# Kernel optimization log

Measured on AMD Instinct MI355X. Metric: run time of the kernel, lower is better.

The kernel has to match this reference:

```python
import jax, jax.numpy as jnp
import numpy as np

K = 15.0          # sigmoid sharpness in get_approxi
THETA2 = 400.0    # gaussian 'theta2' parameter
LOSS_WEIGHT = 1.0


def obb2poly_le90(boxes):
    # boxes [..., 5] = (x, y, w, h, a) -> poly [..., 8]
    x, y, w, h, a = (boxes[..., i] for i in range(5))
    cosa, sina = jnp.cos(a), jnp.sin(a)
    wx, wy = 0.5 * w * cosa, 0.5 * w * sina
    hx, hy = -0.5 * h * sina, 0.5 * h * cosa
    return jnp.stack([
        x - wx - hx, y - wy - hy,
        x + wx - hx, y + wy - hy,
        x + wx + hx, y + wy + hy,
        x - wx + hx, y - wy + hy,
    ], axis=-1)


def setup_inputs() -> dict:
    key = jax.random.key(0)
    k1, k2, k3, k4, k5, k6 = jax.random.split(key, 6)
    N, M = 256, 512

    def make_boxes(k):
        u = jax.random.uniform(k, (N, 5), dtype=jnp.float32)
        cx = 100.0 + 300.0 * u[:, 0]
        cy = 100.0 + 300.0 * u[:, 1]
        w = 20.0 + 100.0 * u[:, 2]
        h = 20.0 + 100.0 * u[:, 3]
        a = (u[:, 4] - 0.5) * (jnp.pi / 2)
        return jnp.stack([cx, cy, w, h, a], axis=-1)

    pred = make_boxes(k1)
    target = make_boxes(k2)
    mask = 512.0 * jax.random.uniform(k3, (N, M, 2), dtype=jnp.float32)
    grad_x = jax.random.normal(k4, (N, M), dtype=jnp.float32)
    grad_y = jax.random.normal(k5, (N, M), dtype=jnp.float32)
    offset = 50.0 * jax.random.uniform(k6, (N, 2), dtype=jnp.float32)
    return {"pred": pred, "target": target, "mask": mask,
            "grad_x": grad_x, "grad_y": grad_y, "offset": offset}


def _my_loss(pred, target, mask, grad_x, grad_y, offset):
    # pred/target [N,5], mask [N,M,2], grad_x/grad_y [N,M], offset [N,2]
    px = pred[:, 0] - offset[:, 0]   # [N]
    py = pred[:, 1] - offset[:, 1]
    pw, ph, pa = pred[:, 2], pred[:, 3], pred[:, 4]
    gx = target[:, 0] - offset[:, 0]
    gy = target[:, 1] - offset[:, 1]
    gw, gh, ga = target[:, 2], target[:, 3], target[:, 4]

    mx, my = mask[..., 0], mask[..., 1]            # [N,M]
    dx = mx - gx[:, None]
    dy = my - gy[:, None]
    d = jnp.sqrt(dx * dx + dy * dy)                # [N,M]
    acos_arg = jnp.clip((gx[:, None] - mx) / d, -1.0, 1.0)
    acosv = jnp.arccos(acos_arg)
    beta = jnp.where(gy[:, None] >= my, ga[:, None] + acosv, ga[:, None] - acosv)

    d_w = jnp.abs(d * jnp.cos(beta))
    d_h = jnp.abs(d * jnp.sin(beta))
    sig = jax.nn.sigmoid
    approxi_1 = (1.0 - sig(K * (d_w - gw[:, None]) / gw[:, None])) * \
                (1.0 - sig(K * (d_h - gh[:, None]) / gh[:, None]))  # [N,M]

    d_w_p = pw[:, None] * d_w / gw[:, None]
    d_h_p = ph[:, None] * d_h / gh[:, None]
    zeros = jnp.zeros_like(d_w_p)
    boxes = jnp.stack([zeros, zeros, 2.0 * d_w_p, 2.0 * d_h_p,
                       jnp.broadcast_to(pa[:, None], d_w_p.shape)], axis=-1)
    pts = obb2poly_le90(boxes)                     # [N,M,8]

    half_pi = jnp.pi / 2
    q2 = (beta > -half_pi) & (beta <= 0.0)
    q3 = (beta > -jnp.pi) & (beta <= -half_pi)
    q4 = (beta > half_pi) & (beta <= jnp.pi)
    # default (q1: 0 < beta <= pi/2) -> corner 0
    gpx = jnp.where(q2, pts[..., 2], jnp.where(q3, pts[..., 4], jnp.where(q4, pts[..., 6], pts[..., 0])))
    gpy = jnp.where(q2, pts[..., 3], jnp.where(q3, pts[..., 5], jnp.where(q4, pts[..., 7], pts[..., 1])))
    guass_x = px[:, None] + gpx                    # [N,M]
    guass_y = py[:, None] + gpy

    # approxi_2[n,i,j] = exp(+||guass_i - mask_j||^2 / (2*theta2^2)) / (2*pi*theta2)
    dgx = guass_x[:, :, None] - mx[:, None, :]
    dgy = guass_y[:, :, None] - my[:, None, :]
    approxi_2 = jnp.exp((dgx * dgx + dgy * dgy) / (2.0 * THETA2 * THETA2)) / (2.0 * jnp.pi * THETA2)

    # w[n,i,j] = gx_i*gx_j + gy_i*gy_j
    w = grad_x[:, :, None] * grad_x[:, None, :] + grad_y[:, :, None] * grad_y[:, None, :]

    loss_per_box = jnp.mean(w * approxi_2 * approxi_1[:, None, :], axis=(1, 2))  # [N]
    return loss_per_box


def reference(pred, target, mask, grad_x, grad_y, offset):
    loss_per_box = _my_loss(pred, target, mask, grad_x, grad_y, offset)
    return LOSS_WEIGHT * jnp.mean(loss_per_box)  # reduction='mean'
```

## Files before the change

### kernel.cpp

```cpp
#include <hip/hip_runtime.h>
#include <math.h>

#define N_BOX 256
#define M_PTS 512
#define SPLIT 2

__global__ __launch_bounds__(256, 2) void loss_kernel(
    const float* __restrict__ pred,
    const float* __restrict__ target,
    const float* __restrict__ mask,
    const float* __restrict__ gradx,
    const float* __restrict__ grady,
    const float* __restrict__ offset,
    float* __restrict__ out)
{
    __shared__ float4 sPack[M_PTS];
    __shared__ float  sWave[4];

    const int n    = blockIdx.x & (N_BOX - 1);
    const int half = blockIdx.x >> 8;
    const int t    = threadIdx.x;

    const float offx = offset[n * 2 + 0];
    const float offy = offset[n * 2 + 1];
    const float px = pred[n * 5 + 0] - offx;
    const float py = pred[n * 5 + 1] - offy;
    const float pw = pred[n * 5 + 2];
    const float ph = pred[n * 5 + 3];
    const float pa = pred[n * 5 + 4];
    const float gx = target[n * 5 + 0] - offx;
    const float gy = target[n * 5 + 1] - offy;
    const float gw = target[n * 5 + 2];
    const float gh = target[n * 5 + 3];
    const float ga = target[n * 5 + 4];

    float sinpa, cospa;
    sincosf(pa, &sinpa, &cospa);

    const float KC       = 15.0f;
    const float THETA2   = 400.0f;
    const float inv_norm = 1.0f / (2.0f * (float)M_PI * THETA2);
    const float PI  = (float)M_PI;
    const float HPI = (float)M_PI * 0.5f;

    float G1x = 0.0f, G1y = 0.0f, g1x = 0.0f, g1y = 0.0f;
#pragma unroll
    for (int j = 0; j < 2; ++j) {
        const int m = t + j * 256;
        const float mx = mask[((size_t)n * M_PTS + m) * 2 + 0];
        const float my = mask[((size_t)n * M_PTS + m) * 2 + 1];
        const float dx = mx - gx;
        const float dy = my - gy;
        const float d  = sqrtf(dx * dx + dy * dy);
        float aa = (gx - mx) / d;
        aa = fminf(1.0f, fmaxf(-1.0f, aa));
        const float ac   = acosf(aa);
        const float beta = (gy >= my) ? (ga + ac) : (ga - ac);
        float sb, cb;
        sincosf(beta, &sb, &cb);
        const float d_w = fabsf(d * cb);
        const float d_h = fabsf(d * sb);
        const float s1  = 1.0f / (1.0f + expf(-(KC * (d_w - gw) / gw)));
        const float s2  = 1.0f / (1.0f + expf(-(KC * (d_h - gh) / gh)));
        const float a1  = (1.0f - s1) * (1.0f - s2);
        const float dwp = pw * d_w / gw;
        const float dhp = ph * d_h / gh;
        const float wx = dwp * cospa, wy = dwp * sinpa;
        const float hx = -dhp * sinpa, hy = dhp * cospa;
        float gpx, gpy;
        if (beta > -HPI && beta <= 0.0f)        { gpx =  wx - hx; gpy =  wy - hy; }
        else if (beta > -PI && beta <= -HPI)    { gpx =  wx + hx; gpy =  wy + hy; }
        else if (beta >  HPI && beta <=  PI)    { gpx = -wx + hx; gpy = -wy + hy; }
        else                                    { gpx = -wx - hx; gpy = -wy - hy; }
        const float gX  = px + gpx;
        const float gY  = py + gpy;
        const float gvx = gradx[(size_t)n * M_PTS + m];
        const float gvy = grady[(size_t)n * M_PTS + m];
        const float B   = a1 * inv_norm;
        sPack[m] = make_float4(mx, my, gvx * B, gvy * B);
        if (j == half) { G1x = gX; G1y = gY; g1x = gvx; g1y = gvy; }
    }
    __syncthreads();

    const float c1 = 1.4426950408889634f / (2.0f * THETA2 * THETA2);
    float acc = 0.0f;
#pragma unroll 8
    for (int m2 = 0; m2 < M_PTS; ++m2) {
        const float4 p = sPack[m2];
        const float dgx = G1x - p.x;
        const float dgy = G1y - p.y;
        const float s   = fmaf(dgy, dgy, dgx * dgx);
        const float e   = exp2f(s * c1);
        const float w   = fmaf(g1y, p.w, g1x * p.z);
        acc = fmaf(w, e, acc);
    }

#pragma unroll
    for (int off = 32; off > 0; off >>= 1)
        acc += __shfl_down(acc, off, 64);
    if ((t & 63) == 0) sWave[t >> 6] = acc;
    __syncthreads();
    if (t == 0) {
        const float tot = sWave[0] + sWave[1] + sWave[2] + sWave[3];
        const float scale = 1.0f / ((float)N_BOX * (float)M_PTS * (float)M_PTS);
        atomicAdd(out, tot * scale);
    }
}

extern "C" void kernel_launch(void* const* d_in, const int* in_sizes, int n_in,
                              void* d_out, int out_size, void* d_ws, size_t ws_size,
                              hipStream_t stream) {
    const float* pred   = (const float*)d_in[0];
    const float* target = (const float*)d_in[1];
    const float* mask   = (const float*)d_in[2];
    const float* gradx  = (const float*)d_in[3];
    const float* grady  = (const float*)d_in[4];
    const float* offset = (const float*)d_in[5];
    float* out = (float*)d_out;

    hipMemsetAsync(out, 0, sizeof(float), stream);
    hipLaunchKernelGGL(loss_kernel, dim3(N_BOX * SPLIT), dim3(256), 0, stream,
                       pred, target, mask, gradx, grady, offset, out);
}
```

Baseline: 93.79 us.

## Rewrite loss kernel with trig-free corner selection, register row tiling, two-stage reduction

Replaces the acos/sincos beta computation with an algebraic rotation into the target box frame plus sign logic for quadrant selection, and computes the sigmoid weights with hardware exp2. Each 64-thread block now keeps 8 rows per thread in packed float2 registers and streams one 64-column slice of the mask from shared memory, pre-scaling coordinates by sqrt(c1) so the multiply inside exp2 disappears. The grad-weighted products are factored out of the inner loop into two accumulators per row. The memset and atomicAdd are replaced by per-block partial sums in the workspace and a separate reduction kernel. This trades an extra launch and duplicated per-row prologue work across the 8 splits for far fewer transcendental calls and more register reuse, and the wrap-around quadrant logic may disagree with the original at boundary cases.

```diff
diff --git a/kernel.cpp b/kernel.cpp
--- a/kernel.cpp
+++ b/kernel.cpp
@@ -1,25 +1,30 @@
 #include <hip/hip_runtime.h>
 #include <math.h>
 
-#define N_BOX 256
-#define M_PTS 512
-#define SPLIT 2
+typedef float v2f __attribute__((ext_vector_type(2)));
 
-__global__ __launch_bounds__(256, 2) void loss_kernel(
+#define N_BOX   256
+#define M_PTS   512
+#define S_SPLIT 8
+#define BLK     64
+#define R_ROWS  8
+#define M2_PER  (M_PTS / S_SPLIT)
+#define GRID    (N_BOX * S_SPLIT)
+
+__global__ __launch_bounds__(BLK, 2) void loss_main(
     const float* __restrict__ pred,
     const float* __restrict__ target,
     const float* __restrict__ mask,
     const float* __restrict__ gradx,
     const float* __restrict__ grady,
     const float* __restrict__ offset,
-    float* __restrict__ out)
+    float* __restrict__ part)
 {
-    __shared__ float4 sPack[M_PTS];
-    __shared__ float  sWave[4];
+    __shared__ float4 sPack[M2_PER];
 
-    const int n    = blockIdx.x & (N_BOX - 1);
-    const int half = blockIdx.x >> 8;
-    const int t    = threadIdx.x;
+    const int n = blockIdx.x >> 3;
+    const int s = blockIdx.x & 7;
+    const int t = threadIdx.x;
 
     const float offx = offset[n * 2 + 0];
     const float offy = offset[n * 2 + 1];
@@ -34,76 +39,110 @@
     const float gh = target[n * 5 + 3];
     const float ga = target[n * 5 + 4];
 
-    float sinpa, cospa;
+    float sinpa, cospa, singa, cosga;
     sincosf(pa, &sinpa, &cospa);
+    sincosf(ga, &singa, &cosga);
 
-    const float KC       = 15.0f;
     const float THETA2   = 400.0f;
+    const float LOG2E    = 1.4426950408889634f;
+    const float c1       = LOG2E / (2.0f * THETA2 * THETA2);
+    const float rs       = sqrtf(c1);
     const float inv_norm = 1.0f / (2.0f * (float)M_PI * THETA2);
-    const float PI  = (float)M_PI;
-    const float HPI = (float)M_PI * 0.5f;
 
-    float G1x = 0.0f, G1y = 0.0f, g1x = 0.0f, g1y = 0.0f;
+    const float pwg = pw / gw, phg = ph / gh;
+    const float cwx = pwg * cospa, swx = pwg * sinpa;
+    const float chx = phg * cospa, shx = phg * sinpa;
+    const float absinga = fabsf(singa);
+    const float kA  = 15.0f * LOG2E / gw;
+    const float kH  = 15.0f * LOG2E / gh;
+    const float kB  = 15.0f * LOG2E;
+    const float pxrs = px * rs, pyrs = py * rs;
+    const bool  gaPos = (ga > 0.0f), gaNeg = (ga < 0.0f);
+
+    const float2* mask2 = (const float2*)mask;
+    const size_t  baseM = (size_t)n * M_PTS;
+
+    v2f Gx[4], Gy[4], gvx2[4], gvy2[4];
+
 #pragma unroll
-    for (int j = 0; j < 2; ++j) {
-        const int m = t + j * 256;
-        const float mx = mask[((size_t)n * M_PTS + m) * 2 + 0];
-        const float my = mask[((size_t)n * M_PTS + m) * 2 + 1];
-        const float dx = mx - gx;
-        const float dy = my - gy;
-        const float d  = sqrtf(dx * dx + dy * dy);
-        float aa = (gx - mx) / d;
-        aa = fminf(1.0f, fmaxf(-1.0f, aa));
-        const float ac   = acosf(aa);
-        const float beta = (gy >= my) ? (ga + ac) : (ga - ac);
-        float sb, cb;
-        sincosf(beta, &sb, &cb);
-        const float d_w = fabsf(d * cb);
-        const float d_h = fabsf(d * sb);
-        const float s1  = 1.0f / (1.0f + expf(-(KC * (d_w - gw) / gw)));
-        const float s2  = 1.0f / (1.0f + expf(-(KC * (d_h - gh) / gh)));
-        const float a1  = (1.0f - s1) * (1.0f - s2);
-        const float dwp = pw * d_w / gw;
-        const float dhp = ph * d_h / gh;
-        const float wx = dwp * cospa, wy = dwp * sinpa;
-        const float hx = -dhp * sinpa, hy = dhp * cospa;
-        float gpx, gpy;
-        if (beta > -HPI && beta <= 0.0f)        { gpx =  wx - hx; gpy =  wy - hy; }
-        else if (beta > -PI && beta <= -HPI)    { gpx =  wx + hx; gpy =  wy + hy; }
-        else if (beta >  HPI && beta <=  PI)    { gpx = -wx + hx; gpy = -wy + hy; }
-        else                                    { gpx = -wx - hx; gpy = -wy - hy; }
-        const float gX  = px + gpx;
-        const float gY  = py + gpy;
-        const float gvx = gradx[(size_t)n * M_PTS + m];
-        const float gvy = grady[(size_t)n * M_PTS + m];
-        const float B   = a1 * inv_norm;
-        sPack[m] = make_float4(mx, my, gvx * B, gvy * B);
-        if (j == half) { G1x = gX; G1y = gY; g1x = gvx; g1y = gvy; }
+    for (int r = 0; r < R_ROWS; ++r) {
+        const int    m  = t + (r << 6);
+        const float2 mp = mask2[baseM + m];
+        const float dx = mp.x - gx;
+        const float dy = mp.y - gy;
+        const float u = singa * dy - cosga * dx;
+        const float v = -(cosga * dy + singa * dx);
+        const bool sgaOk = gaPos ? (dy <= 0.0f) : (gaNeg ? (dy > 0.0f) : false);
+        const bool wrap  = sgaOk && (dx > 0.0f) && (dx * absinga > fabsf(dy) * cosga);
+        const float au = fabsf(u), av = fabsf(v);
+        const float dws = (wrap || v > 0.0f) ? -au : au;
+        const float dhs = (wrap || u > 0.0f) ? -av : av;
+        const float gpx = dws * cwx - dhs * shx;
+        const float gpy = dws * swx + dhs * chx;
+        const float gvx = gradx[baseM + m];
+        const float gvy = grady[baseM + m];
+        Gx[r >> 1][r & 1]   = fmaf(gpx, rs, pxrs);
+        Gy[r >> 1][r & 1]   = fmaf(gpy, rs, pyrs);
+        gvx2[r >> 1][r & 1] = gvx;
+        gvy2[r >> 1][r & 1] = gvy;
+        if (r == s) {
+            const float eA = __builtin_amdgcn_exp2f(fmaf(au, kA, -kB));
+            const float eB = __builtin_amdgcn_exp2f(fmaf(av, kH, -kB));
+            const float B  = inv_norm / ((1.0f + eA) * (1.0f + eB));
+            sPack[t] = make_float4(mp.x * rs, mp.y * rs, gvx * B, gvy * B);
+        }
     }
     __syncthreads();
 
-    const float c1 = 1.4426950408889634f / (2.0f * THETA2 * THETA2);
-    float acc = 0.0f;
-#pragma unroll 8
-    for (int m2 = 0; m2 < M_PTS; ++m2) {
+    v2f accz[4], accw[4];
+#pragma unroll
+    for (int q = 0; q < 4; ++q) { accz[q] = (v2f)0.0f; accw[q] = (v2f)0.0f; }
+
+#pragma unroll 4
+    for (int m2 = 0; m2 < M2_PER; ++m2) {
         const float4 p = sPack[m2];
-        const float dgx = G1x - p.x;
-        const float dgy = G1y - p.y;
-        const float s   = fmaf(dgy, dgy, dgx * dgx);
-        const float e   = exp2f(s * c1);
-        const float w   = fmaf(g1y, p.w, g1x * p.z);
-        acc = fmaf(w, e, acc);
+#pragma unroll
+        for (int q = 0; q < 4; ++q) {
+            v2f dgx = Gx[q] - p.x;
+            v2f dgy = Gy[q] - p.y;
+            v2f sa  = dgx * dgx + dgy * dgy;
+            v2f e;
+            e.x = __builtin_amdgcn_exp2f(sa.x);
+            e.y = __builtin_amdgcn_exp2f(sa.y);
+            accz[q] += e * p.z;
+            accw[q] += e * p.w;
+        }
     }
+
+    v2f tot2 = accz[0] * gvx2[0] + accw[0] * gvy2[0];
+    tot2 += accz[1] * gvx2[1] + accw[1] * gvy2[1];
+    tot2 += accz[2] * gvx2[2] + accw[2] * gvy2[2];
+    tot2 += accz[3] * gvx2[3] + accw[3] * gvy2[3];
+    float acc = tot2.x + tot2.y;
 
 #pragma unroll
     for (int off = 32; off > 0; off >>= 1)
         acc += __shfl_down(acc, off, 64);
-    if ((t & 63) == 0) sWave[t >> 6] = acc;
+    if (t == 0) part[blockIdx.x] = acc;
+}
+
+__global__ __launch_bounds__(256) void loss_reduce(const float* __restrict__ part,
+                                                   float* __restrict__ out)
+{
+    __shared__ float sW[4];
+    const int t = threadIdx.x;
+    const float4* p4 = (const float4*)part;
+    const float4 a = p4[t];
+    const float4 b = p4[t + 256];
+    float acc = ((a.x + a.y) + (a.z + a.w)) + ((b.x + b.y) + (b.z + b.w));
+#pragma unroll
+    for (int off = 32; off > 0; off >>= 1)
+        acc += __shfl_down(acc, off, 64);
+    if ((t & 63) == 0) sW[t >> 6] = acc;
     __syncthreads();
     if (t == 0) {
-        const float tot = sWave[0] + sWave[1] + sWave[2] + sWave[3];
         const float scale = 1.0f / ((float)N_BOX * (float)M_PTS * (float)M_PTS);
-        atomicAdd(out, tot * scale);
+        out[0] = (sW[0] + sW[1] + sW[2] + sW[3]) * scale;
     }
 }
 
@@ -116,9 +155,10 @@
     const float* gradx  = (const float*)d_in[3];
     const float* grady  = (const float*)d_in[4];
     const float* offset = (const float*)d_in[5];
-    float* out = (float*)d_out;
+    float* out  = (float*)d_out;
+    float* part = (float*)d_ws;
 
-    hipMemsetAsync(out, 0, sizeof(float), stream);
-    hipLaunchKernelGGL(loss_kernel, dim3(N_BOX * SPLIT), dim3(256), 0, stream,
-                       pred, target, mask, gradx, grady, offset, out);
+    hipLaunchKernelGGL(loss_main, dim3(GRID), dim3(BLK), 0, stream,
+                       pred, target, mask, gradx, grady, offset, part);
+    hipLaunchKernelGGL(loss_reduce, dim3(1), dim3(256), 0, stream, part, out);
 }
```

Measured after the change: 81.23 us. 1.15x faster.
